# Performance work log

Measured on AMD Instinct MI355X. Metric: run time of the kernel, lower is better.

Reference implementation:

```python
import jax, jax.numpy as jnp
import numpy as np

N_NODES = 100000
N_EDGES = 1600000
D = 128


def _graph_conv(x, src, dst, norm_src, norm_dst, W, b):
    # DGL GraphConv, norm='both': out = D_dst^{-1/2} A D_src^{-1/2} x W + b
    xs = x * norm_src[:, None]                 # [N, d] scale by src (out-)degree
    agg = jax.ops.segment_sum(xs[src], dst, num_segments=N_NODES)  # SpMM
    hd = agg * norm_dst[:, None]
    return hd @ W + b


def setup_inputs() -> dict:
    key = jax.random.key(0)
    ks = jax.random.split(key, 9)
    h = jax.random.normal(ks[0], (N_NODES, D), dtype=jnp.float32)
    src = jax.random.randint(ks[1], (N_EDGES,), 0, N_NODES, dtype=jnp.int64)
    dst = jax.random.randint(ks[2], (N_EDGES,), 0, N_NODES, dtype=jnp.int64)
    s = 1.0 / np.sqrt(D)
    W0 = jax.random.uniform(ks[3], (D, D), jnp.float32, -s, s)
    b0 = jnp.zeros((D,), jnp.float32)
    W1 = jax.random.uniform(ks[4], (D, D), jnp.float32, -s, s)
    b1 = jnp.zeros((D,), jnp.float32)
    W2 = jax.random.uniform(ks[5], (D, D), jnp.float32, -s, s)
    b2 = jnp.zeros((D,), jnp.float32)
    return {"h": h, "src": src, "dst": dst, "W0": W0, "b0": b0,
            "W1": W1, "b1": b1, "W2": W2, "b2": b2}


def reference(h, src, dst, W0, b0, W1, b1, W2, b2):
    ones = jnp.ones((N_EDGES,), jnp.float32)
    deg_out = jnp.maximum(jax.ops.segment_sum(ones, src, num_segments=N_NODES), 1.0)
    deg_in = jnp.maximum(jax.ops.segment_sum(ones, dst, num_segments=N_NODES), 1.0)
    norm_src = deg_out ** -0.5
    norm_dst = deg_in ** -0.5

    x = jax.nn.relu(_graph_conv(h, src, dst, norm_src, norm_dst, W0, b0))
    x = jax.nn.relu(_graph_conv(x, src, dst, norm_src, norm_dst, W1, b1))
    x = _graph_conv(x, src, dst, norm_src, norm_dst, W2, b2)
    # dgl.mean_nodes over a single graph -> [1, out_size]
    return jnp.mean(x, axis=0, keepdims=True)
```

## Files before the change

kernel.cpp:

```cpp
#include <hip/hip_runtime.h>
#include <hip/hip_fp16.h>

#define N_NODES 100000
#define N_EDGES 1600000
#define D 128
#define SCAN_NB ((N_NODES + 1023) / 1024)
#define CHK 128
#define CHUNK_E (N_EDGES / CHK)
#define QTR_N 25000
#define QTR_U (QTR_N / 4)
#define PP_STRIDE (N_NODES / 4)
#define NSH4 4
#define SH4 (N_NODES / NSH4)
#define SH4_U (SH4 / 4)
#define WR 16
#define WRN (N_NODES / WR)
#define WG 64
#define WGE (N_EDGES / WG)

typedef _Float16 f16x4 __attribute__((ext_vector_type(4)));
typedef _Float16 f16x8 __attribute__((ext_vector_type(8)));
typedef float f32x4 __attribute__((ext_vector_type(4)));
typedef float f32x2 __attribute__((ext_vector_type(2)));

__global__ __launch_bounds__(256) void
k_hist(const int* __restrict__ src, const int* __restrict__ dst,
       unsigned int* __restrict__ pp) {
    __shared__ unsigned int h[QTR_U];
    int b = blockIdx.x;
    int arr = b >> 9, q = (b >> 7) & 3, c = b & (CHK - 1);
    const int* a = arr ? dst : src;
    int lo = q * QTR_N;
    for (int i = threadIdx.x; i < QTR_U; i += 256) h[i] = 0;
    __syncthreads();
    int e0 = c * CHUNK_E;
    for (int i = e0 + threadIdx.x; i < e0 + CHUNK_E; i += 256) {
        int v = a[i] - lo;
        if ((unsigned)v < QTR_N)
            atomicAdd(&h[v >> 2], 1u << ((v & 3) * 8));
    }
    __syncthreads();
    unsigned int* po = pp + ((size_t)(arr * CHK + c)) * PP_STRIDE + q * QTR_U;
    for (int i = threadIdx.x; i < QTR_U; i += 256) po[i] = h[i];
}

__global__ void k_merge(unsigned int* __restrict__ pp,
                        int* __restrict__ cnt_src, int* __restrict__ cnt_dst) {
    int g = blockIdx.x * blockDim.x + threadIdx.x;
    if (g >= 2 * PP_STRIDE) return;
    int arr = g / PP_STRIDE, u = g % PP_STRIDE;
    unsigned int* p = pp + ((size_t)arr * CHK) * PP_STRIDE + u;
    int s0 = 0, s1 = 0, s2 = 0, s3 = 0;
    if (arr == 0) {
#pragma unroll 8
        for (int c = 0; c < CHK; c++) {
            unsigned int v = p[(size_t)c * PP_STRIDE];
            s0 += v & 255; s1 += (v >> 8) & 255; s2 += (v >> 16) & 255; s3 += (v >> 24) & 255;
        }
        cnt_src[4 * u + 0] = s0; cnt_src[4 * u + 1] = s1;
        cnt_src[4 * u + 2] = s2; cnt_src[4 * u + 3] = s3;
    } else {
#pragma unroll 8
        for (int c = 0; c < CHK; c++) {
            unsigned int v = p[(size_t)c * PP_STRIDE];
            p[(size_t)c * PP_STRIDE] =
                (unsigned)s0 | ((unsigned)s1 << 8) | ((unsigned)s2 << 16) | ((unsigned)s3 << 24);
            s0 += v & 255; s1 += (v >> 8) & 255; s2 += (v >> 16) & 255; s3 += (v >> 24) & 255;
        }
        cnt_dst[4 * u + 0] = s0; cnt_dst[4 * u + 1] = s1;
        cnt_dst[4 * u + 2] = s2; cnt_dst[4 * u + 3] = s3;
    }
}

__global__ __launch_bounds__(1024) void
k_scan1(const int* __restrict__ cnt, int* __restrict__ rp1, int* __restrict__ bs) {
    __shared__ int s[1024];
    int tid = threadIdx.x;
    int i = blockIdx.x * 1024 + tid;
    int v = (i < N_NODES) ? cnt[i] : 0;
    s[tid] = v;
    __syncthreads();
    for (int d = 1; d < 1024; d <<= 1) {
        int t = (tid >= d) ? s[tid - d] : 0;
        __syncthreads();
        s[tid] += t;
        __syncthreads();
    }
    if (i < N_NODES) rp1[i] = s[tid];
    if (tid == 1023) bs[blockIdx.x] = s[1023];
}

__global__ void k_scan2(int* __restrict__ bs) {
    __shared__ int s[128];
    int tid = threadIdx.x;
    int v = (tid < SCAN_NB) ? bs[tid] : 0;
    s[tid] = v;
    __syncthreads();
    for (int d = 1; d < 128; d <<= 1) {
        int t = (tid >= d) ? s[tid - d] : 0;
        __syncthreads();
        s[tid] += t;
        __syncthreads();
    }
    if (tid < SCAN_NB) bs[tid] = s[tid] - v;
}

__global__ void k_scan3norm(int* __restrict__ rpD, const int* __restrict__ bsD,
                            const int* __restrict__ cnt_src, const int* __restrict__ cnt_dst,
                            float* __restrict__ ns, float* __restrict__ nd,
                            float* __restrict__ colsum) {
    int i = blockIdx.x * blockDim.x + threadIdx.x;
    if (i >= N_NODES) return;
    rpD[1 + i] += bsD[i >> 10];
    if (i == 0) rpD[0] = 0;
    if (i < 128) colsum[i] = 0.0f;
    ns[i] = rsqrtf((float)max(cnt_src[i], 1));
    nd[i] = rsqrtf((float)max(cnt_dst[i], 1));
}

__global__ __launch_bounds__(256) void
k_scatter_dst(const int* __restrict__ src, const int* __restrict__ dst,
              const int* __restrict__ rpD, const unsigned int* __restrict__ pp,
              int* __restrict__ csr_src) {
    __shared__ unsigned int cur[SH4_U];
    int sh = blockIdx.x & 3, c = blockIdx.x >> 2;
    int lo = sh * SH4;
    const unsigned int* pre = pp + ((size_t)(CHK + c)) * PP_STRIDE;
    for (int i = threadIdx.x; i < SH4_U; i += 256) cur[i] = 0;
    __syncthreads();
    int e0 = c * CHUNK_E;
    for (int i = e0 + threadIdx.x; i < e0 + CHUNK_E; i += 256) {
        int dfull = dst[i];
        int d = dfull - lo;
        if ((unsigned)d < SH4) {
            int sft = (d & 3) * 8;
            int rank = (atomicAdd(&cur[d >> 2], 1u << sft) >> sft) & 255;
            int p8 = (pre[dfull >> 2] >> ((dfull & 3) * 8)) & 255;
            csr_src[rpD[dfull] + p8 + rank] = src[i];
        }
    }
}

__global__ __launch_bounds__(256) void
k_wacc(const int* __restrict__ src, const int* __restrict__ dst,
       const float* __restrict__ nd, float* __restrict__ wpart) {
    __shared__ float acc[WRN];
    int r = blockIdx.x & (WR - 1), g = blockIdx.x >> 4;
    int lo = r * WRN;
    for (int i = threadIdx.x; i < WRN; i += 256) acc[i] = 0.0f;
    __syncthreads();
    int e0 = g * WGE;
    for (int i = e0 + threadIdx.x; i < e0 + WGE; i += 256) {
        int s = src[i] - lo;
        if ((unsigned)s < WRN) atomicAdd(&acc[s], nd[dst[i]]);
    }
    __syncthreads();
    float* po = wpart + ((size_t)g * WR + r) * WRN;
    for (int i = threadIdx.x; i < WRN; i += 256) po[i] = acc[i];
}

__global__ void k_wmerge(const float* __restrict__ wpart, const float* __restrict__ ns,
                         float* __restrict__ wsum) {
    int n = blockIdx.x * blockDim.x + threadIdx.x;
    if (n >= N_NODES) return;
    int r = n / WRN, local = n % WRN;
    float s = 0.0f;
#pragma unroll 8
    for (int g = 0; g < WG; g++)
        s += wpart[((size_t)g * WR + r) * WRN + local];
    wsum[n] = s * ns[n];
}

__global__ void k_prep(const float* __restrict__ W0, const float* __restrict__ W1,
                       __half* __restrict__ Wt, const float* __restrict__ x,
                       const float* __restrict__ ns, unsigned int* __restrict__ out) {
    if (blockIdx.x < 128) {
        int i = blockIdx.x * 256 + threadIdx.x;
        int l = i >> 14, r = i & (D * D - 1);
        int n = r >> 7, k = r & 127;
        const float* W = l ? W1 : W0;
        Wt[i] = __float2half(W[k * D + n]);
        return;
    }
    int i = (blockIdx.x - 128) * 256 + threadIdx.x;
    if (i >= N_NODES * (D / 4)) return;
    int n = i >> 5;
    float4 v = ((const float4*)x)[i];
    float s = ns[n];
    int u = __builtin_amdgcn_cvt_pk_fp8_f32(v.x * s, v.y * s, 0, false);
    u = __builtin_amdgcn_cvt_pk_fp8_f32(v.z * s, v.w * s, u, true);
    out[i] = (unsigned int)u;
}

__global__ __launch_bounds__(256) void
k_spmm(const unsigned char* __restrict__ x8, const int* __restrict__ row_ptr,
       const int* __restrict__ csr_src, __half* __restrict__ agg) {
    int wave = (blockIdx.x * blockDim.x + threadIdx.x) >> 6;
    int lane = threadIdx.x & 63;
    int hf = lane >> 5, l32 = lane & 31;
    if (wave >= N_NODES) return;
    int beg = row_ptr[wave], end = row_ptr[wave + 1];
    float a0 = 0.f, a1 = 0.f, a2 = 0.f, a3 = 0.f;
    int j = beg;
    for (; j + 7 < end; j += 8) {
#pragma unroll
        for (int p = 0; p < 4; p++) {
            int s0 = csr_src[j + 2 * p];
            int s1 = csr_src[j + 2 * p + 1];
            int s = hf ? s1 : s0;
            unsigned int u = *(const unsigned int*)(x8 + (size_t)s * D + 4 * l32);
            f32x2 lo = __builtin_amdgcn_cvt_pk_f32_fp8(u, false);
            f32x2 hi = __builtin_amdgcn_cvt_pk_f32_fp8(u, true);
            a0 += lo[0]; a1 += lo[1]; a2 += hi[0]; a3 += hi[1];
        }
    }
    for (; j + 1 < end; j += 2) {
        int s0 = csr_src[j], s1 = csr_src[j + 1];
        int s = hf ? s1 : s0;
        unsigned int u = *(const unsigned int*)(x8 + (size_t)s * D + 4 * l32);
        f32x2 lo = __builtin_amdgcn_cvt_pk_f32_fp8(u, false);
        f32x2 hi = __builtin_amdgcn_cvt_pk_f32_fp8(u, true);
        a0 += lo[0]; a1 += lo[1]; a2 += hi[0]; a3 += hi[1];
    }
    if (j < end && hf == 0) {
        int s = csr_src[j];
        unsigned int u = *(const unsigned int*)(x8 + (size_t)s * D + 4 * l32);
        f32x2 lo = __builtin_amdgcn_cvt_pk_f32_fp8(u, false);
        f32x2 hi = __builtin_amdgcn_cvt_pk_f32_fp8(u, true);
        a0 += lo[0]; a1 += lo[1]; a2 += hi[0]; a3 += hi[1];
    }
    a0 += __shfl_xor(a0, 32, 64);
    a1 += __shfl_xor(a1, 32, 64);
    a2 += __shfl_xor(a2, 32, 64);
    a3 += __shfl_xor(a3, 32, 64);
    if (hf == 0) {
        f16x4 o;
        o[0] = (_Float16)a0; o[1] = (_Float16)a1; o[2] = (_Float16)a2; o[3] = (_Float16)a3;
        ((f16x4*)(agg + (size_t)wave * D))[l32] = o;
    }
}

__global__ __launch_bounds__(256) void
k_gemm_mfma(const __half* __restrict__ A, const __half* __restrict__ Wt,
            const float* __restrict__ b, const float* __restrict__ nd,
            const float* __restrict__ ns, unsigned char* __restrict__ out) {
    int w = threadIdx.x >> 6, lane = threadIdx.x & 63;
    int m = lane & 15, q = lane >> 4;
    int row0 = blockIdx.x * 128 + w * 32;

    f16x8 zf;
#pragma unroll
    for (int j = 0; j < 8; j++) zf[j] = (_Float16)0;
    f16x8 af[2][4];
#pragma unroll
    for (int g = 0; g < 2; g++) {
        int arow = row0 + g * 16 + m;
        const f16x8* pa = (const f16x8*)(A + (size_t)arow * D);
        bool aok = arow < N_NODES;
#pragma unroll
        for (int ks = 0; ks < 4; ks++) af[g][ks] = aok ? pa[ks * 4 + q] : zf;
    }

    const f16x8* pb = (const f16x8*)Wt;
    f32x4 acc[2][8];
#pragma unroll
    for (int g = 0; g < 2; g++)
#pragma unroll
        for (int nt = 0; nt < 8; nt++) acc[g][nt] = (f32x4){0.f, 0.f, 0.f, 0.f};

#pragma unroll
    for (int ks = 0; ks < 4; ks++) {
#pragma unroll
        for (int nt = 0; nt < 8; nt++) {
            f16x8 bf = pb[((nt * 16 + m) << 4) + (ks << 2) + q];
            acc[0][nt] = __builtin_amdgcn_mfma_f32_16x16x32_f16(af[0][ks], bf, acc[0][nt], 0, 0, 0);
            acc[1][nt] = __builtin_amdgcn_mfma_f32_16x16x32_f16(af[1][ks], bf, acc[1][nt], 0, 0, 0);
        }
    }

#pragma unroll
    for (int g = 0; g < 2; g++) {
        int er = row0 + g * 16 + q * 4;
        float sd[4], ss[4];
#pragma unroll
        for (int r = 0; r < 4; r++) {
            int n = er + r;
            bool ok = n < N_NODES;
            sd[r] = ok ? nd[n] : 0.0f;
            ss[r] = ok ? ns[n] : 0.0f;
        }
#pragma unroll
        for (int nt = 0; nt < 8; nt++) {
            int col = nt * 16 + m;
            float bc = b[col];
#pragma unroll
            for (int r = 0; r < 4; r++) {
                int n = er + r;
                if (n < N_NODES) {
                    float v = fmaxf(sd[r] * acc[g][nt][r] + bc, 0.0f) * ss[r];
                    int pk = __builtin_amdgcn_cvt_pk_fp8_f32(v, v, 0, false);
                    out[(size_t)n * D + col] = (unsigned char)(pk & 0xff);
                }
            }
        }
    }
}

__global__ __launch_bounds__(256) void
k_gemm_red(const __half* __restrict__ A, const __half* __restrict__ Wt,
           const float* __restrict__ b, const float* __restrict__ nd,
           const float* __restrict__ wsum, float* __restrict__ colsum) {
    __shared__ float red[128];
    int tid = threadIdx.x;
    if (tid < 128) red[tid] = 0.0f;
    __syncthreads();

    int w = tid >> 6, lane = tid & 63;
    int m = lane & 15, q = lane >> 4;
    int row0 = blockIdx.x * 128 + w * 32;

    f16x8 zf;
#pragma unroll
    for (int j = 0; j < 8; j++) zf[j] = (_Float16)0;
    f16x8 af[2][4];
#pragma unroll
    for (int g = 0; g < 2; g++) {
        int arow = row0 + g * 16 + m;
        const f16x8* pa = (const f16x8*)(A + (size_t)arow * D);
        bool aok = arow < N_NODES;
#pragma unroll
        for (int ks = 0; ks < 4; ks++) af[g][ks] = aok ? pa[ks * 4 + q] : zf;
    }

    const f16x8* pb = (const f16x8*)Wt;
    f32x4 acc[2][8];
#pragma unroll
    for (int g = 0; g < 2; g++)
#pragma unroll
        for (int nt = 0; nt < 8; nt++) acc[g][nt] = (f32x4){0.f, 0.f, 0.f, 0.f};

#pragma unroll
    for (int ks = 0; ks < 4; ks++) {
#pragma unroll
        for (int nt = 0; nt < 8; nt++) {
            f16x8 bf = pb[((nt * 16 + m) << 4) + (ks << 2) + q];
            acc[0][nt] = __builtin_amdgcn_mfma_f32_16x16x32_f16(af[0][ks], bf, acc[0][nt], 0, 0, 0);
            acc[1][nt] = __builtin_amdgcn_mfma_f32_16x16x32_f16(af[1][ks], bf, acc[1][nt], 0, 0, 0);
        }
    }

    float sd[2][4], sw[2][4];
#pragma unroll
    for (int g = 0; g < 2; g++) {
        int er = row0 + g * 16 + q * 4;
#pragma unroll
        for (int r = 0; r < 4; r++) {
            int n = er + r;
            bool ok = n < N_NODES;
            sd[g][r] = ok ? nd[n] : 0.0f;
            sw[g][r] = ok ? wsum[n] : 0.0f;
        }
    }
#pragma unroll
    for (int nt = 0; nt < 8; nt++) {
        int col = nt * 16 + m;
        float bc = b[col];
        float pc = 0.0f;
#pragma unroll
        for (int g = 0; g < 2; g++)
#pragma unroll
            for (int r = 0; r < 4; r++)
                pc += sw[g][r] * fmaxf(sd[g][r] * acc[g][nt][r] + bc, 0.0f);
        atomicAdd(&red[col], pc);
    }
    __syncthreads();
    if (tid < 128) unsafeAtomicAdd(&colsum[tid], red[tid]);
}

__global__ void k_final(const float* __restrict__ colsum, const float* __restrict__ W,
                        const float* __restrict__ b, float* __restrict__ out) {
    __shared__ float m[128];
    int j = threadIdx.x;
    m[j] = colsum[j] * (1.0f / N_NODES);
    __syncthreads();
    float acc = b[j];
    for (int k = 0; k < 128; k++)
        acc = fmaf(m[k], W[(size_t)k * D + j], acc);
    out[j] = acc;
}

extern "C" void kernel_launch(void* const* d_in, const int* in_sizes, int n_in,
                              void* d_out, int out_size, void* d_ws, size_t ws_size,
                              hipStream_t stream) {
    const float* h   = (const float*)d_in[0];
    const int*   src = (const int*)d_in[1];
    const int*   dst = (const int*)d_in[2];
    const float* W0  = (const float*)d_in[3];
    const float* b0  = (const float*)d_in[4];
    const float* W1  = (const float*)d_in[5];
    const float* b1  = (const float*)d_in[6];
    const float* W2  = (const float*)d_in[7];
    const float* b2  = (const float*)d_in[8];
    float* out = (float*)d_out;

    float*         ns      = (float*)d_ws;
    float*         nd      = ns + N_NODES;
    float*         wsum    = nd + N_NODES;
    float*         colsum  = wsum + N_NODES;
    int*           rpD     = (int*)(colsum + 128);
    int*           cnt_src = rpD + N_NODES + 1;
    int*           cnt_dst = cnt_src + N_NODES;
    int*           bsD     = cnt_dst + N_NODES;
    __half*        Wt16    = (__half*)(bsD + 128);
    int*           csr_src = (int*)(Wt16 + 2 * D * D);
    float*         wpart   = (float*)(csr_src + N_EDGES);
    unsigned int*  pp      = (unsigned int*)(wpart + (size_t)WG * WR * WRN);
    unsigned char* x8      = (unsigned char*)pp;
    __half*        agg16   = (__half*)(pp + 2 * (size_t)CHK * PP_STRIDE);

    k_hist<<<2 * 4 * CHK, 256, 0, stream>>>(src, dst, pp);
    k_merge<<<(2 * PP_STRIDE + 255) / 256, 256, 0, stream>>>(pp, cnt_src, cnt_dst);
    k_scan1<<<SCAN_NB, 1024, 0, stream>>>(cnt_dst, rpD + 1, bsD);
    k_scan2<<<1, 128, 0, stream>>>(bsD);
    k_scan3norm<<<(N_NODES + 255) / 256, 256, 0, stream>>>(rpD, bsD, cnt_src, cnt_dst,
                                                           ns, nd, colsum);
    k_scatter_dst<<<NSH4 * CHK, 256, 0, stream>>>(src, dst, rpD, pp, csr_src);
    k_wacc<<<WG * WR, 256, 0, stream>>>(src, dst, nd, wpart);
    k_wmerge<<<(N_NODES + 255) / 256, 256, 0, stream>>>(wpart, ns, wsum);

    k_prep<<<128 + (N_NODES * (D / 4) + 255) / 256, 256, 0, stream>>>(
        W0, W1, Wt16, h, ns, (unsigned int*)x8);

    k_spmm<<<(N_NODES + 3) / 4, 256, 0, stream>>>(x8, rpD, csr_src, agg16);
    k_gemm_mfma<<<(N_NODES + 127) / 128, 256, 0, stream>>>(agg16, Wt16, b0, nd, ns, x8);
    k_spmm<<<(N_NODES + 3) / 4, 256, 0, stream>>>(x8, rpD, csr_src, agg16);
    k_gemm_red<<<(N_NODES + 127) / 128, 256, 0, stream>>>(agg16, Wt16 + (size_t)D * D,
                                                          b1, nd, wsum, colsum);
    k_final<<<1, 128, 0, stream>>>(colsum, W2, b2, out);
}
```

Before: 472.5 us.

## Fuse source-degree counting into the weight-accumulation pass and drop the src histogram

Source out-degree counts are now computed inside k_wacc, which already streams src, using packed byte counters in LDS. k_wmerge then derives the norm_src value and wsum together. The separate src histogram pass and its merge are removed, and the dst histogram is repartitioned into 8 node ranges. This saves one full read of the edge array plus the partial histogram traffic, at the cost of more range blocks (WR=40) and an extra shared atomic per edge in k_wacc.

```diff
diff --git a/kernel.cpp b/kernel.cpp
--- a/kernel.cpp
+++ b/kernel.cpp
@@ -7,14 +7,16 @@
 #define SCAN_NB ((N_NODES + 1023) / 1024)
 #define CHK 128
 #define CHUNK_E (N_EDGES / CHK)
-#define QTR_N 25000
-#define QTR_U (QTR_N / 4)
+#define HR 8
+#define HRN (N_NODES / HR)
+#define HRU (HRN / 4)
 #define PP_STRIDE (N_NODES / 4)
 #define NSH4 4
 #define SH4 (N_NODES / NSH4)
 #define SH4_U (SH4 / 4)
-#define WR 16
+#define WR 40
 #define WRN (N_NODES / WR)
+#define WRU (WRN / 4)
 #define WG 64
 #define WGE (N_EDGES / WG)
 
@@ -24,52 +26,37 @@
 typedef float f32x2 __attribute__((ext_vector_type(2)));
 
 __global__ __launch_bounds__(256) void
-k_hist(const int* __restrict__ src, const int* __restrict__ dst,
-       unsigned int* __restrict__ pp) {
-    __shared__ unsigned int h[QTR_U];
-    int b = blockIdx.x;
-    int arr = b >> 9, q = (b >> 7) & 3, c = b & (CHK - 1);
-    const int* a = arr ? dst : src;
-    int lo = q * QTR_N;
-    for (int i = threadIdx.x; i < QTR_U; i += 256) h[i] = 0;
+k_hist(const int* __restrict__ dst, unsigned int* __restrict__ pp) {
+    __shared__ unsigned int h[HRU];
+    int r = blockIdx.x >> 7, c = blockIdx.x & (CHK - 1);
+    int lo = r * HRN;
+    for (int i = threadIdx.x; i < HRU; i += 256) h[i] = 0;
     __syncthreads();
     int e0 = c * CHUNK_E;
     for (int i = e0 + threadIdx.x; i < e0 + CHUNK_E; i += 256) {
-        int v = a[i] - lo;
-        if ((unsigned)v < QTR_N)
+        int v = dst[i] - lo;
+        if ((unsigned)v < HRN)
             atomicAdd(&h[v >> 2], 1u << ((v & 3) * 8));
     }
     __syncthreads();
-    unsigned int* po = pp + ((size_t)(arr * CHK + c)) * PP_STRIDE + q * QTR_U;
-    for (int i = threadIdx.x; i < QTR_U; i += 256) po[i] = h[i];
-}
-
-__global__ void k_merge(unsigned int* __restrict__ pp,
-                        int* __restrict__ cnt_src, int* __restrict__ cnt_dst) {
-    int g = blockIdx.x * blockDim.x + threadIdx.x;
-    if (g >= 2 * PP_STRIDE) return;
-    int arr = g / PP_STRIDE, u = g % PP_STRIDE;
-    unsigned int* p = pp + ((size_t)arr * CHK) * PP_STRIDE + u;
+    unsigned int* po = pp + (size_t)c * PP_STRIDE + r * HRU;
+    for (int i = threadIdx.x; i < HRU; i += 256) po[i] = h[i];
+}
+
+__global__ void k_merge(unsigned int* __restrict__ pp, int* __restrict__ cnt_dst) {
+    int u = blockIdx.x * blockDim.x + threadIdx.x;
+    if (u >= PP_STRIDE) return;
+    unsigned int* p = pp + u;
     int s0 = 0, s1 = 0, s2 = 0, s3 = 0;
-    if (arr == 0) {
 #pragma unroll 8
-        for (int c = 0; c < CHK; c++) {
-            unsigned int v = p[(size_t)c * PP_STRIDE];
-            s0 += v & 255; s1 += (v >> 8) & 255; s2 += (v >> 16) & 255; s3 += (v >> 24) & 255;
-        }
-        cnt_src[4 * u + 0] = s0; cnt_src[4 * u + 1] = s1;
-        cnt_src[4 * u + 2] = s2; cnt_src[4 * u + 3] = s3;
-    } else {
-#pragma unroll 8
-        for (int c = 0; c < CHK; c++) {
-            unsigned int v = p[(size_t)c * PP_STRIDE];
-            p[(size_t)c * PP_STRIDE] =
-                (unsigned)s0 | ((unsigned)s1 << 8) | ((unsigned)s2 << 16) | ((unsigned)s3 << 24);
-            s0 += v & 255; s1 += (v >> 8) & 255; s2 += (v >> 16) & 255; s3 += (v >> 24) & 255;
-        }
-        cnt_dst[4 * u + 0] = s0; cnt_dst[4 * u + 1] = s1;
-        cnt_dst[4 * u + 2] = s2; cnt_dst[4 * u + 3] = s3;
-    }
+    for (int c = 0; c < CHK; c++) {
+        unsigned int v = p[(size_t)c * PP_STRIDE];
+        p[(size_t)c * PP_STRIDE] =
+            (unsigned)s0 | ((unsigned)s1 << 8) | ((unsigned)s2 << 16) | ((unsigned)s3 << 24);
+        s0 += v & 255; s1 += (v >> 8) & 255; s2 += (v >> 16) & 255; s3 += (v >> 24) & 255;
+    }
+    cnt_dst[4 * u + 0] = s0; cnt_dst[4 * u + 1] = s1;
+    cnt_dst[4 * u + 2] = s2; cnt_dst[4 * u + 3] = s3;
 }
 
 __global__ __launch_bounds__(1024) void
@@ -105,16 +92,14 @@
     if (tid < SCAN_NB) bs[tid] = s[tid] - v;
 }
 
-__global__ void k_scan3norm(int* __restrict__ rpD, const int* __restrict__ bsD,
-                            const int* __restrict__ cnt_src, const int* __restrict__ cnt_dst,
-                            float* __restrict__ ns, float* __restrict__ nd,
-                            float* __restrict__ colsum) {
+__global__ void k_scan3nd(int* __restrict__ rpD, const int* __restrict__ bsD,
+                          const int* __restrict__ cnt_dst,
+                          float* __restrict__ nd, float* __restrict__ colsum) {
     int i = blockIdx.x * blockDim.x + threadIdx.x;
     if (i >= N_NODES) return;
     rpD[1 + i] += bsD[i >> 10];
     if (i == 0) rpD[0] = 0;
     if (i < 128) colsum[i] = 0.0f;
-    ns[i] = rsqrtf((float)max(cnt_src[i], 1));
     nd[i] = rsqrtf((float)max(cnt_dst[i], 1));
 }
 
@@ -125,7 +110,7 @@
     __shared__ unsigned int cur[SH4_U];
     int sh = blockIdx.x & 3, c = blockIdx.x >> 2;
     int lo = sh * SH4;
-    const unsigned int* pre = pp + ((size_t)(CHK + c)) * PP_STRIDE;
+    const unsigned int* pre = pp + (size_t)c * PP_STRIDE;
     for (int i = threadIdx.x; i < SH4_U; i += 256) cur[i] = 0;
     __syncthreads();
     int e0 = c * CHUNK_E;
@@ -143,32 +128,46 @@
 
 __global__ __launch_bounds__(256) void
 k_wacc(const int* __restrict__ src, const int* __restrict__ dst,
-       const float* __restrict__ nd, float* __restrict__ wpart) {
+       const float* __restrict__ nd, float* __restrict__ wpart,
+       unsigned int* __restrict__ cpart) {
     __shared__ float acc[WRN];
-    int r = blockIdx.x & (WR - 1), g = blockIdx.x >> 4;
+    __shared__ unsigned int cnt[WRU];
+    int r = blockIdx.x % WR, g = blockIdx.x / WR;
     int lo = r * WRN;
     for (int i = threadIdx.x; i < WRN; i += 256) acc[i] = 0.0f;
+    for (int i = threadIdx.x; i < WRU; i += 256) cnt[i] = 0;
     __syncthreads();
     int e0 = g * WGE;
     for (int i = e0 + threadIdx.x; i < e0 + WGE; i += 256) {
         int s = src[i] - lo;
-        if ((unsigned)s < WRN) atomicAdd(&acc[s], nd[dst[i]]);
-    }
-    __syncthreads();
-    float* po = wpart + ((size_t)g * WR + r) * WRN;
+        if ((unsigned)s < WRN) {
+            atomicAdd(&acc[s], nd[dst[i]]);
+            atomicAdd(&cnt[s >> 2], 1u << ((s & 3) * 8));
+        }
+    }
+    __syncthreads();
+    float* po = wpart + (size_t)g * N_NODES + lo;
     for (int i = threadIdx.x; i < WRN; i += 256) po[i] = acc[i];
-}
-
-__global__ void k_wmerge(const float* __restrict__ wpart, const float* __restrict__ ns,
-                         float* __restrict__ wsum) {
+    unsigned int* co = cpart + (size_t)g * (N_NODES / 4) + (lo >> 2);
+    for (int i = threadIdx.x; i < WRU; i += 256) co[i] = cnt[i];
+}
+
+__global__ void k_wmerge(const float* __restrict__ wpart,
+                         const unsigned int* __restrict__ cpart,
+                         float* __restrict__ ns, float* __restrict__ wsum) {
     int n = blockIdx.x * blockDim.x + threadIdx.x;
     if (n >= N_NODES) return;
-    int r = n / WRN, local = n % WRN;
     float s = 0.0f;
+    int c = 0;
+    int sft = (n & 3) * 8;
 #pragma unroll 8
-    for (int g = 0; g < WG; g++)
-        s += wpart[((size_t)g * WR + r) * WRN + local];
-    wsum[n] = s * ns[n];
+    for (int g = 0; g < WG; g++) {
+        s += wpart[(size_t)g * N_NODES + n];
+        c += (cpart[(size_t)g * (N_NODES / 4) + (n >> 2)] >> sft) & 255;
+    }
+    float nsv = rsqrtf((float)max(c, 1));
+    ns[n] = nsv;
+    wsum[n] = s * nsv;
 }
 
 __global__ void k_prep(const float* __restrict__ W0, const float* __restrict__ W1,
@@ -408,25 +407,24 @@
     float*         wsum    = nd + N_NODES;
     float*         colsum  = wsum + N_NODES;
     int*           rpD     = (int*)(colsum + 128);
-    int*           cnt_src = rpD + N_NODES + 1;
-    int*           cnt_dst = cnt_src + N_NODES;
+    int*           cnt_dst = rpD + N_NODES + 1;
     int*           bsD     = cnt_dst + N_NODES;
     __half*        Wt16    = (__half*)(bsD + 128);
     int*           csr_src = (int*)(Wt16 + 2 * D * D);
     float*         wpart   = (float*)(csr_src + N_EDGES);
-    unsigned int*  pp      = (unsigned int*)(wpart + (size_t)WG * WR * WRN);
+    unsigned int*  cpart   = (unsigned int*)(wpart + (size_t)WG * N_NODES);
+    unsigned int*  pp      = cpart + (size_t)WG * (N_NODES / 4);
     unsigned char* x8      = (unsigned char*)pp;
-    __half*        agg16   = (__half*)(pp + 2 * (size_t)CHK * PP_STRIDE);
-
-    k_hist<<<2 * 4 * CHK, 256, 0, stream>>>(src, dst, pp);
-    k_merge<<<(2 * PP_STRIDE + 255) / 256, 256, 0, stream>>>(pp, cnt_src, cnt_dst);
+    __half*        agg16   = (__half*)(pp + (size_t)CHK * PP_STRIDE);
+
+    k_hist<<<HR * CHK, 256, 0, stream>>>(dst, pp);
+    k_merge<<<(PP_STRIDE + 255) / 256, 256, 0, stream>>>(pp, cnt_dst);
     k_scan1<<<SCAN_NB, 1024, 0, stream>>>(cnt_dst, rpD + 1, bsD);
     k_scan2<<<1, 128, 0, stream>>>(bsD);
-    k_scan3norm<<<(N_NODES + 255) / 256, 256, 0, stream>>>(rpD, bsD, cnt_src, cnt_dst,
-                                                           ns, nd, colsum);
+    k_scan3nd<<<(N_NODES + 255) / 256, 256, 0, stream>>>(rpD, bsD, cnt_dst, nd, colsum);
     k_scatter_dst<<<NSH4 * CHK, 256, 0, stream>>>(src, dst, rpD, pp, csr_src);
-    k_wacc<<<WG * WR, 256, 0, stream>>>(src, dst, nd, wpart);
-    k_wmerge<<<(N_NODES + 255) / 256, 256, 0, stream>>>(wpart, ns, wsum);
+    k_wacc<<<WR * WG, 256, 0, stream>>>(src, dst, nd, wpart, cpart);
+    k_wmerge<<<(N_NODES + 255) / 256, 256, 0, stream>>>(wpart, cpart, ns, wsum);
 
     k_prep<<<128 + (N_NODES * (D / 4) + 255) / 256, 256, 0, stream>>>(
         W0, W1, Wt16, h, ns, (unsigned int*)x8);
```

After: 511.6 us. +8.3%, slower.
